# Kernel optimization log

Hardware: AMD Instinct MI355X
Metric: run time of the kernel (lower is better)

Reference implementation:

```python
import jax, jax.numpy as jnp
import numpy as np

N_NODES = 100000
N_EDGES = 1600000
D_FEAT = 64


def setup_inputs() -> dict:
    key = jax.random.key(0)
    k1, k2, k3 = jax.random.split(key, 3)
    x = jax.random.normal(k1, (N_NODES, D_FEAT), dtype=jnp.float32)
    neighbor_idx = jax.random.randint(k2, (N_EDGES,), 0, N_NODES, dtype=jnp.int64)
    segment_ids = jnp.sort(jax.random.randint(k3, (N_EDGES,), 0, N_NODES, dtype=jnp.int64))
    return {"x": x, "neighbor_idx": neighbor_idx, "segment_ids": segment_ids}


def reference(x, neighbor_idx, segment_ids):
    # Flattened-CSR equivalent of the per-node loop:
    #   pooled[i] = max over neighbors j of node i of x[j], or zeros if no neighbors.
    n = x.shape[0]
    gathered = x[neighbor_idx]  # [E, d] gather
    pooled = jax.ops.segment_max(gathered, segment_ids, num_segments=n,
                                 indices_are_sorted=True)  # [N, d]; -inf for empty segments
    counts = jax.ops.segment_sum(jnp.ones((segment_ids.shape[0],), dtype=jnp.int32),
                                 segment_ids, num_segments=n, indices_are_sorted=True)
    # Nodes with no neighbors get zeros, matching torch.zeros_like(x[0]).
    return jnp.where(counts[:, None] > 0, pooled, jnp.zeros((), dtype=x.dtype))
```

## Files before the change

### kernel.cpp

```cpp
#include <hip/hip_runtime.h>
#include <math.h>

#define D_FEAT 64

__global__ void build_starts_kernel(const int* __restrict__ seg,
                                    int* __restrict__ starts,
                                    int nE, int nN) {
    int e = blockIdx.x * blockDim.x + threadIdx.x;
    if (e >= nE) return;
    int s = seg[e];
    int sprev = (e == 0) ? -1 : seg[e - 1];
    for (int v = sprev + 1; v <= s; ++v) starts[v] = e;
    if (e == nE - 1) {
        for (int v = s + 1; v <= nN; ++v) starts[v] = nE;
    }
}

__device__ __forceinline__ int lower_bound_dev(const int* __restrict__ seg,
                                               int nE, int val) {
    int lo = 0, hi = nE;
    while (lo < hi) {
        int mid = (lo + hi) >> 1;
        if (seg[mid] < val) lo = mid + 1; else hi = mid;
    }
    return lo;
}

template<bool USE_STARTS>
__global__ __launch_bounds__(256) void seg_max_kernel(
    const float* __restrict__ x, const int* __restrict__ nbr,
    const int* __restrict__ seg, const int* __restrict__ starts,
    float* __restrict__ out, int nE, int nN) {
    int wid  = blockIdx.x * (blockDim.x >> 6) + (threadIdx.x >> 6);
    int lane = threadIdx.x & 63;
    if (wid >= nN) return;

    int s, e;
    if (USE_STARTS) {
        s = __builtin_amdgcn_readfirstlane(starts[wid]);
        e = __builtin_amdgcn_readfirstlane(starts[wid + 1]);
    } else {
        s = __builtin_amdgcn_readfirstlane(lower_bound_dev(seg, nE, wid));
        e = __builtin_amdgcn_readfirstlane(lower_bound_dev(seg, nE, wid + 1));
    }

    if (e <= s) {
        __builtin_nontemporal_store(0.0f, out + wid * D_FEAT + lane);
        return;
    }

    const float* __restrict__ xl = x + lane;
    const int eM1 = e - 1;
    float m = -INFINITY;

    for (int k = s; k < e; k += 64) {
        int kc = k + lane;
        kc = (kc < eM1) ? kc : eM1;
        int idxv = __builtin_nontemporal_load(nbr + kc);

#pragma unroll
        for (int j0 = 0; j0 < 64; j0 += 16) {
            if (k + j0 < e) {
                float val[16];
#pragma unroll
                for (int j = 0; j < 16; ++j) {
                    int rj = __builtin_amdgcn_readlane(idxv, j0 + j);
                    const float* __restrict__ row = x + ((size_t)rj << 6);
                    val[j] = row[lane];
                }
                float t0 = fmaxf(fmaxf(val[0], val[1]), fmaxf(val[2], val[3]));
                float t1 = fmaxf(fmaxf(val[4], val[5]), fmaxf(val[6], val[7]));
                float t2 = fmaxf(fmaxf(val[8], val[9]), fmaxf(val[10], val[11]));
                float t3 = fmaxf(fmaxf(val[12], val[13]), fmaxf(val[14], val[15]));
                m = fmaxf(m, fmaxf(fmaxf(t0, t1), fmaxf(t2, t3)));
            }
        }
    }

    __builtin_nontemporal_store(m, out + wid * D_FEAT + lane);
    (void)xl;
}

extern "C" void kernel_launch(void* const* d_in, const int* in_sizes, int n_in,
                              void* d_out, int out_size, void* d_ws, size_t ws_size,
                              hipStream_t stream) {
    const float* x   = (const float*)d_in[0];
    const int*   nbr = (const int*)d_in[1];
    const int*   seg = (const int*)d_in[2];
    float*       out = (float*)d_out;

    int nN = in_sizes[0] / D_FEAT;
    int nE = in_sizes[1];

    const int wavesPerBlock = 4;
    int grid = (nN + wavesPerBlock - 1) / wavesPerBlock;

    size_t starts_bytes = (size_t)(nN + 1) * sizeof(int);
    if (ws_size >= starts_bytes) {
        int* starts = (int*)d_ws;
        int bgrid = (nE + 255) / 256;
        hipLaunchKernelGGL(build_starts_kernel, dim3(bgrid), dim3(256), 0, stream,
                           seg, starts, nE, nN);
        hipLaunchKernelGGL((seg_max_kernel<true>), dim3(grid), dim3(256), 0, stream,
                           x, nbr, seg, starts, out, nE, nN);
    } else {
        hipLaunchKernelGGL((seg_max_kernel<false>), dim3(grid), dim3(256), 0, stream,
                           x, nbr, seg, nullptr, out, nE, nN);
    }
}
```

Measured before the change: 133.0 us.

## Use float4 row gathers with 4 rows per wave and persistent grid-stride waves

The wave is split into 4 groups of 16 lanes, and each group loads a different neighbor row as float4, so one load instruction fetches 4 rows instead of 1. Partial maxima are combined across the groups with xor shuffles. The kernel also becomes persistent: a fixed 2048-block grid strides over nodes and prefetches the next node's segment bounds. This cuts per-row instruction count and launch overhead, at the cost of a cross-group reduction per node and possibly less latency hiding from the smaller grid.

Result: slower. 138.8 us (+4.4%).

```diff
diff --git a/kernel.cpp b/kernel.cpp
--- a/kernel.cpp
+++ b/kernel.cpp
@@ -2,6 +2,7 @@
 #include <math.h>
 
 #define D_FEAT 64
+typedef float f32x4 __attribute__((ext_vector_type(4)));
 
 __global__ void build_starts_kernel(const int* __restrict__ seg,
                                     int* __restrict__ starts,
@@ -30,55 +31,82 @@
 __global__ __launch_bounds__(256) void seg_max_kernel(
     const float* __restrict__ x, const int* __restrict__ nbr,
     const int* __restrict__ seg, const int* __restrict__ starts,
-    float* __restrict__ out, int nE, int nN) {
+    float* __restrict__ out, int nE, int nN, int nWaves) {
     int wid  = blockIdx.x * (blockDim.x >> 6) + (threadIdx.x >> 6);
     int lane = threadIdx.x & 63;
-    if (wid >= nN) return;
+    int g    = lane >> 4;
+    int sub  = lane & 15;
+    size_t feat_off = (size_t)sub * 4;
+
+    int v = wid;
+    if (v >= nN) return;
 
     int s, e;
     if (USE_STARTS) {
-        s = __builtin_amdgcn_readfirstlane(starts[wid]);
-        e = __builtin_amdgcn_readfirstlane(starts[wid + 1]);
+        s = __builtin_amdgcn_readfirstlane(starts[v]);
+        e = __builtin_amdgcn_readfirstlane(starts[v + 1]);
     } else {
-        s = __builtin_amdgcn_readfirstlane(lower_bound_dev(seg, nE, wid));
-        e = __builtin_amdgcn_readfirstlane(lower_bound_dev(seg, nE, wid + 1));
+        s = __builtin_amdgcn_readfirstlane(lower_bound_dev(seg, nE, v));
+        e = __builtin_amdgcn_readfirstlane(lower_bound_dev(seg, nE, v + 1));
     }
 
-    if (e <= s) {
-        __builtin_nontemporal_store(0.0f, out + wid * D_FEAT + lane);
-        return;
-    }
-
-    const float* __restrict__ xl = x + lane;
-    const int eM1 = e - 1;
-    float m = -INFINITY;
-
-    for (int k = s; k < e; k += 64) {
-        int kc = k + lane;
-        kc = (kc < eM1) ? kc : eM1;
-        int idxv = __builtin_nontemporal_load(nbr + kc);
-
-#pragma unroll
-        for (int j0 = 0; j0 < 64; j0 += 16) {
-            if (k + j0 < e) {
-                float val[16];
-#pragma unroll
-                for (int j = 0; j < 16; ++j) {
-                    int rj = __builtin_amdgcn_readlane(idxv, j0 + j);
-                    const float* __restrict__ row = x + ((size_t)rj << 6);
-                    val[j] = row[lane];
-                }
-                float t0 = fmaxf(fmaxf(val[0], val[1]), fmaxf(val[2], val[3]));
-                float t1 = fmaxf(fmaxf(val[4], val[5]), fmaxf(val[6], val[7]));
-                float t2 = fmaxf(fmaxf(val[8], val[9]), fmaxf(val[10], val[11]));
-                float t3 = fmaxf(fmaxf(val[12], val[13]), fmaxf(val[14], val[15]));
-                m = fmaxf(m, fmaxf(fmaxf(t0, t1), fmaxf(t2, t3)));
+    while (v < nN) {
+        int vn = v + nWaves;
+        int sn = 0, en = 0;
+        if (vn < nN) {
+            if (USE_STARTS) {
+                sn = __builtin_amdgcn_readfirstlane(starts[vn]);
+                en = __builtin_amdgcn_readfirstlane(starts[vn + 1]);
+            } else {
+                sn = __builtin_amdgcn_readfirstlane(lower_bound_dev(seg, nE, vn));
+                en = __builtin_amdgcn_readfirstlane(lower_bound_dev(seg, nE, vn + 1));
             }
         }
+
+        f32x4 m;
+        if (e > s) {
+            m.x = m.y = m.z = m.w = -INFINITY;
+            const int eM1 = e - 1;
+            for (int k = s; k < e; k += 64) {
+                int kc = k + lane;
+                kc = (kc < eM1) ? kc : eM1;
+                int idxv = __builtin_nontemporal_load(nbr + kc);
+#pragma unroll
+                for (int q = 0; q < 16; ++q) {
+                    if (k + 4 * q < e) {
+                        int row = __shfl(idxv, 4 * q + g, 64);
+                        const f32x4* rp = (const f32x4*)(x + ((size_t)row << 6) + feat_off);
+                        f32x4 val = *rp;
+                        m.x = fmaxf(m.x, val.x);
+                        m.y = fmaxf(m.y, val.y);
+                        m.z = fmaxf(m.z, val.z);
+                        m.w = fmaxf(m.w, val.w);
+                    }
+                }
+            }
+#pragma unroll
+            for (int off = 16; off < 64; off <<= 1) {
+                f32x4 o;
+                o.x = __shfl_xor(m.x, off, 64);
+                o.y = __shfl_xor(m.y, off, 64);
+                o.z = __shfl_xor(m.z, off, 64);
+                o.w = __shfl_xor(m.w, off, 64);
+                m.x = fmaxf(m.x, o.x);
+                m.y = fmaxf(m.y, o.y);
+                m.z = fmaxf(m.z, o.z);
+                m.w = fmaxf(m.w, o.w);
+            }
+        } else {
+            m.x = m.y = m.z = m.w = 0.0f;
+        }
+
+        if (g == 0) {
+            __builtin_nontemporal_store(m,
+                (f32x4*)(out + (size_t)v * D_FEAT + feat_off));
+        }
+
+        v = vn; s = sn; e = en;
     }
-
-    __builtin_nontemporal_store(m, out + wid * D_FEAT + lane);
-    (void)xl;
 }
 
 extern "C" void kernel_launch(void* const* d_in, const int* in_sizes, int n_in,
@@ -93,7 +121,8 @@
     int nE = in_sizes[1];
 
     const int wavesPerBlock = 4;
-    int grid = (nN + wavesPerBlock - 1) / wavesPerBlock;
+    int grid = 2048;
+    int nWaves = grid * wavesPerBlock;
 
     size_t starts_bytes = (size_t)(nN + 1) * sizeof(int);
     if (ws_size >= starts_bytes) {
@@ -102,9 +131,9 @@
         hipLaunchKernelGGL(build_starts_kernel, dim3(bgrid), dim3(256), 0, stream,
                            seg, starts, nE, nN);
         hipLaunchKernelGGL((seg_max_kernel<true>), dim3(grid), dim3(256), 0, stream,
-                           x, nbr, seg, starts, out, nE, nN);
+                           x, nbr, seg, starts, out, nE, nN, nWaves);
     } else {
         hipLaunchKernelGGL((seg_max_kernel<false>), dim3(grid), dim3(256), 0, stream,
-                           x, nbr, seg, nullptr, out, nE, nN);
+                           x, nbr, seg, nullptr, out, nE, nN, nWaves);
     }
 }
```

## Process four consecutive segments per wave with prefetched neighbor indices

Applied to the files above, without the earlier changes.

Each wavefront now handles a run of four consecutive nodes instead of one. It loads all segment bounds with a single vector load and prefetches the next segment's neighbor indices while reducing the current one. The gather granularity drops from 16 rows to 4 rows per step, which cuts wasted work on short segments (about 16 edges on average) but exposes less memory-level parallelism per wave. With four times fewer waves, occupancy and latency hiding may suffer.

Result: slower. 139.7 us (+5.1%).

```diff
diff --git a/kernel.cpp b/kernel.cpp
--- a/kernel.cpp
+++ b/kernel.cpp
@@ -2,6 +2,7 @@
 #include <math.h>
 
 #define D_FEAT 64
+#define RUN 4
 
 __global__ void build_starts_kernel(const int* __restrict__ seg,
                                     int* __restrict__ starts,
@@ -33,52 +34,68 @@
     float* __restrict__ out, int nE, int nN) {
     int wid  = blockIdx.x * (blockDim.x >> 6) + (threadIdx.x >> 6);
     int lane = threadIdx.x & 63;
-    if (wid >= nN) return;
+    int v0 = wid * RUN;
+    if (v0 >= nN) return;
+    int nrun = (nN - v0 < RUN) ? (nN - v0) : RUN;
 
-    int s, e;
+    int bl = 0;
     if (USE_STARTS) {
-        s = __builtin_amdgcn_readfirstlane(starts[wid]);
-        e = __builtin_amdgcn_readfirstlane(starts[wid + 1]);
+        if (lane <= nrun) bl = starts[v0 + lane];
     } else {
-        s = __builtin_amdgcn_readfirstlane(lower_bound_dev(seg, nE, wid));
-        e = __builtin_amdgcn_readfirstlane(lower_bound_dev(seg, nE, wid + 1));
+        if (lane <= nrun) bl = lower_bound_dev(seg, nE, v0 + lane);
     }
 
-    if (e <= s) {
-        __builtin_nontemporal_store(0.0f, out + wid * D_FEAT + lane);
-        return;
+    int sC = __builtin_amdgcn_readlane(bl, 0);
+    int eC = __builtin_amdgcn_readlane(bl, 1);
+    int idxC = 0;
+    if (eC > sC) {
+        int kc = sC + lane;
+        kc = (kc < eC - 1) ? kc : (eC - 1);
+        idxC = __builtin_nontemporal_load(nbr + kc);
     }
 
-    const float* __restrict__ xl = x + lane;
-    const int eM1 = e - 1;
-    float m = -INFINITY;
-
-    for (int k = s; k < e; k += 64) {
-        int kc = k + lane;
-        kc = (kc < eM1) ? kc : eM1;
-        int idxv = __builtin_nontemporal_load(nbr + kc);
-
-#pragma unroll
-        for (int j0 = 0; j0 < 64; j0 += 16) {
-            if (k + j0 < e) {
-                float val[16];
-#pragma unroll
-                for (int j = 0; j < 16; ++j) {
-                    int rj = __builtin_amdgcn_readlane(idxv, j0 + j);
-                    const float* __restrict__ row = x + ((size_t)rj << 6);
-                    val[j] = row[lane];
-                }
-                float t0 = fmaxf(fmaxf(val[0], val[1]), fmaxf(val[2], val[3]));
-                float t1 = fmaxf(fmaxf(val[4], val[5]), fmaxf(val[6], val[7]));
-                float t2 = fmaxf(fmaxf(val[8], val[9]), fmaxf(val[10], val[11]));
-                float t3 = fmaxf(fmaxf(val[12], val[13]), fmaxf(val[14], val[15]));
-                m = fmaxf(m, fmaxf(fmaxf(t0, t1), fmaxf(t2, t3)));
+    for (int r = 0; r < nrun; ++r) {
+        int s = sC, e = eC, idxv = idxC;
+        if (r + 1 < nrun) {
+            sC = e;
+            eC = __builtin_amdgcn_readlane(bl, r + 2);
+            if (eC > sC) {
+                int kc = sC + lane;
+                kc = (kc < eC - 1) ? kc : (eC - 1);
+                idxC = __builtin_nontemporal_load(nbr + kc);
             }
         }
+
+        float m;
+        if (e > s) {
+            m = -INFINITY;
+            for (int k = s; k < e; k += 64) {
+                if (k != s) {
+                    int kc = k + lane;
+                    kc = (kc < e - 1) ? kc : (e - 1);
+                    idxv = __builtin_nontemporal_load(nbr + kc);
+                }
+#pragma unroll
+                for (int j0 = 0; j0 < 64; j0 += 4) {
+                    if (k + j0 < e) {
+                        int r0 = __builtin_amdgcn_readlane(idxv, j0 + 0);
+                        int r1 = __builtin_amdgcn_readlane(idxv, j0 + 1);
+                        int r2 = __builtin_amdgcn_readlane(idxv, j0 + 2);
+                        int r3 = __builtin_amdgcn_readlane(idxv, j0 + 3);
+                        float a = x[((size_t)r0 << 6) + lane];
+                        float b = x[((size_t)r1 << 6) + lane];
+                        float c = x[((size_t)r2 << 6) + lane];
+                        float d = x[((size_t)r3 << 6) + lane];
+                        m = fmaxf(m, fmaxf(fmaxf(a, b), fmaxf(c, d)));
+                    }
+                }
+            }
+        } else {
+            m = 0.0f;
+        }
+
+        __builtin_nontemporal_store(m, out + (size_t)(v0 + r) * D_FEAT + lane);
     }
-
-    __builtin_nontemporal_store(m, out + wid * D_FEAT + lane);
-    (void)xl;
 }
 
 extern "C" void kernel_launch(void* const* d_in, const int* in_sizes, int n_in,
@@ -93,7 +110,8 @@
     int nE = in_sizes[1];
 
     const int wavesPerBlock = 4;
-    int grid = (nN + wavesPerBlock - 1) / wavesPerBlock;
+    int nWaves = (nN + RUN - 1) / RUN;
+    int grid = (nWaves + wavesPerBlock - 1) / wavesPerBlock;
 
     size_t starts_bytes = (size_t)(nN + 1) * sizeof(int);
     if (ws_size >= starts_bytes) {
```
